# Kernel optimization log

Hardware: AMD Instinct MI355X
Metric: run time of the kernel (lower is better)

Reference implementation:

```python
import jax, jax.numpy as jnp
import numpy as np

B, S, D, H, ROT = 2, 2048, 2048, 16, 64
HD = D // H  # 128


def setup_inputs() -> dict:
    key = jax.random.key(0)
    ks = jax.random.split(key, 6)
    sc = 0.02
    return {
        "hidden_states": jax.random.normal(ks[0], (B, S, D), jnp.float32),
        "attention_mask": jnp.zeros((B, 1, 1, S), jnp.float32),  # HF additive mask; 0 == keep
        "position_ids": jnp.tile(jnp.arange(S, dtype=jnp.int32), (B, 1)),
        "Wq": jax.random.normal(ks[1], (D, D), jnp.float32) * sc,
        "Wk": jax.random.normal(ks[2], (D, D), jnp.float32) * sc,
        "Wv": jax.random.normal(ks[3], (D, D), jnp.float32) * sc,
        "Wo": jax.random.normal(ks[4], (D, D), jnp.float32) * sc,
        "norm_const": 0.5 * jnp.ones((1, H, 1, 1), jnp.float32),
    }


def _rotate_every_two(x):
    x1 = x[..., ::2]
    x2 = x[..., 1::2]
    return jnp.stack((-x2, x1), axis=-1).reshape(x.shape)


def _apply_rope(x, sin, cos):
    # x: [B,S,H,ROT]; sin/cos: [B,S,ROT//2] -> repeat_interleave(2) as in GPT-J
    sin2 = jnp.repeat(sin, 2, axis=-1)[:, :, None, :]
    cos2 = jnp.repeat(cos, 2, axis=-1)[:, :, None, :]
    return x * cos2 + _rotate_every_two(x) * sin2


def reference(hidden_states, attention_mask, position_ids, Wq, Wk, Wv, Wo, norm_const):
    # projections (nn.Linear, no bias): y = x @ W^T
    q = (hidden_states @ Wq.T).reshape(B, S, H, HD)
    k = (hidden_states @ Wk.T).reshape(B, S, H, HD)
    v = (hidden_states @ Wv.T).reshape(B, S, H, HD).transpose(0, 2, 1, 3)  # [B,H,S,HD]

    # GPT-J sinusoidal rotary on first ROT dims
    inv_freq = 1.0 / (10000.0 ** (jnp.arange(0, ROT, 2, dtype=jnp.float32) / ROT))
    ang = position_ids.astype(jnp.float32)[:, :, None] * inv_freq  # [B,S,ROT//2]
    sin, cos = jnp.sin(ang), jnp.cos(ang)
    q = jnp.concatenate([_apply_rope(q[..., :ROT], sin, cos), q[..., ROT:]], axis=-1)
    k = jnp.concatenate([_apply_rope(k[..., :ROT], sin, cos), k[..., ROT:]], axis=-1)
    q = q.transpose(0, 2, 1, 3)  # [B,H,S,HD]
    k = k.transpose(0, 2, 1, 3)

    # cosine attention: L2-normalize q and k (F.normalize, eps=1e-12)
    eps = 1e-12
    qn = q / jnp.clip(jnp.linalg.norm(q, axis=-1, keepdims=True), eps)
    kn = k / jnp.clip(jnp.linalg.norm(k, axis=-1, keepdims=True), eps)

    keep = attention_mask == 0                               # [B,1,1,S] bool
    causal = jnp.tril(jnp.ones((S, S), bool))[None, None]    # [1,1,S,S]
    # per-query count of visible keys -> value rescale with learned exponent
    counts = jnp.sum((causal & keep).astype(jnp.float32), axis=-1, keepdims=True)  # [B,1,S,1]
    expo = jax.nn.sigmoid(norm_const)                        # [1,H,1,1]
    v = v / jnp.clip(counts ** expo, 1.0)                    # [B,H,S,HD]

    keep_t = jnp.swapaxes(keep, -1, -2).astype(q.dtype)      # [B,1,S,1]
    qn = qn * keep_t
    kn = kn * keep_t
    v = v * keep_t

    attn = jnp.einsum('bhqd,bhkd->bhqk', qn, kn)             # cosine scores
    attn = jnp.where(causal, attn, 0.0)                      # causal zero-mask (no softmax)
    out = jnp.einsum('bhqk,bhkd->bhqd', attn, v)             # [B,H,S,HD]
    out = out.transpose(0, 2, 1, 3).reshape(B, S, D)
    return out @ Wo.T
```

## Files before the change

kernel.cpp:

```cpp
#include <hip/hip_runtime.h>
#include <hip/hip_bf16.h>

typedef __attribute__((ext_vector_type(8))) short bf16x8;
typedef __attribute__((ext_vector_type(4))) float f32x4;
typedef unsigned short u16;
typedef unsigned int u32;

constexpr int B = 2, S = 2048, D = 2048, H = 16, HD = 128, ROT = 64;
constexpr int NQKV = 3 * D;

__device__ __forceinline__ void gload16(const u16* g, u16* l)
{
    __builtin_amdgcn_global_load_lds((const __attribute__((address_space(1))) void*)g,
                                     (__attribute__((address_space(3))) void*)l, 16, 0, 0);
}

__device__ __forceinline__ float bf2f(u32 lo16) { return __uint_as_float(lo16 << 16); }

__global__ void fused_prep(const float* __restrict__ hs,
                           const float* __restrict__ Wq, const float* __restrict__ Wk,
                           const float* __restrict__ Wv, const float* __restrict__ Wo,
                           const float* __restrict__ mask, const int* __restrict__ pos,
                           const float* __restrict__ ncst,
                           u16* __restrict__ hs16, u16* __restrict__ wqkv16, u16* __restrict__ wo16,
                           float2* __restrict__ sc2, float* __restrict__ keep,
                           float* __restrict__ expo, float* __restrict__ counts)
{
    int bid = blockIdx.x, tid = threadIdx.x;
    if (bid < 1024) {
        const int total = 2097152 + 4 * 1048576;
        int idx = bid * 256 + tid;
        int stride = 1024 * 256;
        for (int i = idx; i < total; i += stride) {
            const float* src; u16* dst; int off;
            if (i < 2097152) { src = hs; dst = hs16; off = i; }
            else {
                int j = i - 2097152;
                int wsel = j >> 20; off = j & 1048575;
                src = wsel == 0 ? Wq : wsel == 1 ? Wk : wsel == 2 ? Wv : Wo;
                dst = wsel < 3 ? wqkv16 + (size_t)wsel * D * D : wo16;
            }
            float4 v = ((const float4*)src)[off];
            __hip_bfloat16 a = __float2bfloat16(v.x);
            __hip_bfloat16 b = __float2bfloat16(v.y);
            __hip_bfloat16 c = __float2bfloat16(v.z);
            __hip_bfloat16 d = __float2bfloat16(v.w);
            ushort4 o;
            o.x = *(u16*)&a; o.y = *(u16*)&b; o.z = *(u16*)&c; o.w = *(u16*)&d;
            ((ushort4*)dst)[off] = o;
        }
    } else if (bid < 1536) {
        int gid = (bid - 1024) * 256 + tid;
        int j = gid & 31;
        int bs = gid >> 5;
        float p = (float)pos[bs];
        float f = powf(10000.f, -(float)j / 32.f);
        float ang = p * f;
        sc2[gid] = make_float2(cosf(ang), sinf(ang));
        if (j == 0) keep[bs] = (mask[bs] == 0.f) ? 1.f : 0.f;
        if (gid < H) expo[gid] = 1.f / (1.f + expf(-ncst[gid]));
    } else {
        __shared__ float part[256];
        int b = bid - 1536, t = tid;
        float v[8];
        float s = 0.f;
        const float* mp = mask + b * S + t * 8;
#pragma unroll
        for (int i = 0; i < 8; ++i) { s += (mp[i] == 0.f) ? 1.f : 0.f; v[i] = s; }
        part[t] = s;
        __syncthreads();
        float off = 0.f;
        for (int j = 0; j < t; ++j) off += part[j];
        float* cp = counts + b * S + t * 8;
#pragma unroll
        for (int i = 0; i < 8; ++i) cp[i] = off + v[i];
    }
}


template <int CNT>
__device__ __forceinline__ void stage_op(const u16* __restrict__ G, int K,
                                         int trow0, int kt, u16* lbuf, int tid)
{
#pragma unroll
    for (int l = 0; l < CNT; ++l) {
        int idx = l * 512 + tid;
        int row = idx >> 2;
        int slot = idx & 3;
        int col8 = slot ^ ((row >> 1) & 3);
        const u16* g = G + (size_t)(trow0 + row) * K + kt * 32 + col8 * 8;
        u16* ld = lbuf + (size_t)(idx & ~63) * 8;
        gload16(g, ld);
    }
}

template <int BM, int BN, int CA, int CB, int MR, int NR, int BF16OUT>
__global__ __launch_bounds__(512, 2) void gemm32(
    const u16* __restrict__ A, const u16* __restrict__ Bm,
    float* __restrict__ Cf, u16* __restrict__ Cb, int N, int K, int ntn)
{
    __shared__ u16 As[3 * BM * 32];
    __shared__ u16 Bs[3 * BN * 32];
    const int tid = threadIdx.x;
    const int lane = tid & 63;
    const int w = tid >> 6;
    const int wm = w >> 2;
    const int wn = w & 3;
    const int l15 = lane & 15, l4 = lane >> 4;

    int nwg = gridDim.x;
    int bid = blockIdx.x;
    int cpx = nwg >> 3;
    int sbid = (bid & 7) * cpx + (bid >> 3);
    int bm = sbid / ntn, bn = sbid % ntn;
    const int bmrow = bm * BM, bnrow = bn * BN;

    f32x4 acc[MR][NR] = {};
    const int nk = K >> 5;

    stage_op<CA>(A, K, bmrow, 0, &As[0], tid);
    stage_op<CB>(Bm, K, bnrow, 0, &Bs[0], tid);
    stage_op<CA>(A, K, bmrow, 1, &As[BM * 32], tid);
    stage_op<CB>(Bm, K, bnrow, 1, &Bs[BN * 32], tid);

    int c0 = 0;
    for (int t = 0; t < nk; ++t) {
        const u16* ab = &As[c0 * BM * 32];
        const u16* bb = &Bs[c0 * BN * 32];
        if (t + 2 < nk) {
            int c2 = c0 + 2; if (c2 >= 3) c2 -= 3;
            stage_op<CA>(A, K, bmrow, t + 2, &As[c2 * BM * 32], tid);
            stage_op<CB>(Bm, K, bnrow, t + 2, &Bs[c2 * BN * 32], tid);
            asm volatile("s_waitcnt vmcnt(%0)" :: "i"(2 * (CA + CB)) : "memory");
        } else if (t + 1 < nk) {
            asm volatile("s_waitcnt vmcnt(%0)" :: "i"(CA + CB) : "memory");
        } else {
            asm volatile("s_waitcnt vmcnt(0)" ::: "memory");
        }
        __builtin_amdgcn_sched_barrier(0);
        __builtin_amdgcn_s_barrier();

        bf16x8 af[MR];
#pragma unroll
        for (int i = 0; i < MR; ++i) {
            int row = wm * (BM / 2) + i * 16 + l15;
            int slot = l4 ^ ((row >> 1) & 3);
            af[i] = *(const bf16x8*)(ab + row * 32 + slot * 8);
        }
#pragma unroll
        for (int n = 0; n < NR; ++n) {
            int brow = wn * (BN / 4) + n * 16 + l15;
            int bslot = l4 ^ ((brow >> 1) & 3);
            bf16x8 bf = *(const bf16x8*)(bb + brow * 32 + bslot * 8);
            __builtin_amdgcn_s_setprio(1);
#pragma unroll
            for (int i = 0; i < MR; ++i)
                acc[i][n] = __builtin_amdgcn_mfma_f32_16x16x32_bf16(af[i], bf, acc[i][n], 0, 0, 0);
            __builtin_amdgcn_s_setprio(0);
        }
        __builtin_amdgcn_sched_barrier(0);
        __builtin_amdgcn_s_barrier();
        c0 = (c0 + 1 == 3) ? 0 : c0 + 1;
    }

#pragma unroll
    for (int i = 0; i < MR; ++i) {
        int row = bmrow + wm * (BM / 2) + i * 16 + l4 * 4;
#pragma unroll
        for (int n = 0; n < NR; ++n) {
            int col = bnrow + wn * (BN / 4) + n * 16 + l15;
            f32x4 v = acc[i][n];
#pragma unroll
            for (int r = 0; r < 4; ++r) {
                if (BF16OUT) {
                    __hip_bfloat16 hv = __float2bfloat16(v[r]);
                    Cb[(size_t)(row + r) * N + col] = *(u16*)&hv;
                } else {
                    Cf[(size_t)(row + r) * N + col] = v[r];
                }
            }
        }
    }
}

__global__ void postproc_all(const u16* __restrict__ tmpb,
                             u16* __restrict__ qn, u16* __restrict__ kn, u16* __restrict__ vr,
                             const float2* __restrict__ sc2,
                             const float* __restrict__ keep, const float* __restrict__ counts,
                             const float* __restrict__ expo)
{
    int gw = (blockIdx.x * blockDim.x + threadIdx.x) >> 6;
    int lane = threadIdx.x & 63;
    if (gw >= B * S * H) return;
    int h = gw % H;
    int sb = gw / H;
    int s = sb % S;
    int b = sb / S;
    const u16* rowp = tmpb + (size_t)(b * S + s) * NQKV;
    u32 qv = *(const u32*)(rowp + h * 128 + lane * 2);
    u32 kv = *(const u32*)(rowp + D + h * 128 + lane * 2);
    u32 vv = *(const u32*)(rowp + 2 * D + h * 128 + lane * 2);
    float q0 = bf2f(qv & 0xffff), q1 = bf2f(qv >> 16);
    float k0 = bf2f(kv & 0xffff), k1 = bf2f(kv >> 16);
    float v0 = bf2f(vv & 0xffff), v1 = bf2f(vv >> 16);
    if (lane < 32) {
        float2 cs = sc2[(b * S + s) * 32 + lane];
        float nq0 = q0 * cs.x - q1 * cs.y, nq1 = q1 * cs.x + q0 * cs.y;
        float nk0 = k0 * cs.x - k1 * cs.y, nk1 = k1 * cs.x + k0 * cs.y;
        q0 = nq0; q1 = nq1; k0 = nk0; k1 = nk1;
    }
    float sq = q0 * q0 + q1 * q1;
    float sk = k0 * k0 + k1 * k1;
#pragma unroll
    for (int o = 1; o < 64; o <<= 1) {
        sq += __shfl_xor(sq, o, 64);
        sk += __shfl_xor(sk, o, 64);
    }
    float kf = keep[b * S + s];
    float scq = kf / fmaxf(sqrtf(sq), 1e-12f);
    float sck = kf / fmaxf(sqrtf(sk), 1e-12f);
    float cnt = counts[b * S + s];
    float e = expo[h];
    float scv = kf / fmaxf(powf(cnt, e), 1.0f);

    __hip_bfloat16 a0 = __float2bfloat16(q0 * scq), a1 = __float2bfloat16(q1 * scq);
    __hip_bfloat16 b0 = __float2bfloat16(k0 * sck), b1 = __float2bfloat16(k1 * sck);
    __hip_bfloat16 c0 = __float2bfloat16(v0 * scv), c1 = __float2bfloat16(v1 * scv);
    size_t obase = ((size_t)(b * H + h) * S + s) * 128 + lane * 2;
    *(u32*)(qn + obase) = (u32)*(u16*)&a0 | ((u32)*(u16*)&a1 << 16);
    *(u32*)(kn + obase) = (u32)*(u16*)&b0 | ((u32)*(u16*)&b1 << 16);
    *(u32*)(vr + obase) = (u32)*(u16*)&c0 | ((u32)*(u16*)&c1 << 16);
}

__global__ __launch_bounds__(256) void chunk_state(
    const u16* __restrict__ kn, const u16* __restrict__ vr, u16* __restrict__ T16)
{
    __shared__ u16 As[128][72];
    __shared__ u16 Bs[128][72];
    int tid = threadIdx.x, lane = tid & 63, w = tid >> 6;
    int wm = w >> 1, wn = w & 1;
    int c = blockIdx.x, bh = blockIdx.y;
    const int l15 = lane & 15, l4 = lane >> 4;
    size_t base = (size_t)bh * S * 128;
    f32x4 acc[4][4] = {};

    for (int t = 0; t < 2; ++t) {
#pragma unroll
        for (int i = 0; i < 4; ++i) {
            int q = tid + i * 256;
            int r = q >> 4, c16 = q & 15;
            uint4 v = *(const uint4*)(vr + base + (size_t)(c * 128 + t * 64 + r) * 128 + c16 * 8);
            const u16* pv = (const u16*)&v;
#pragma unroll
            for (int j = 0; j < 8; ++j) As[c16 * 8 + j][r] = pv[j];
        }
#pragma unroll
        for (int i = 0; i < 4; ++i) {
            int q = tid + i * 256;
            int r = q >> 4, c16 = q & 15;
            uint4 v = *(const uint4*)(kn + base + (size_t)(c * 128 + t * 64 + r) * 128 + c16 * 8);
            const u16* pv = (const u16*)&v;
#pragma unroll
            for (int j = 0; j < 8; ++j) Bs[c16 * 8 + j][r] = pv[j];
        }
        __syncthreads();
#pragma unroll
        for (int tt = 0; tt < 2; ++tt) {
            bf16x8 a[4], b[4];
#pragma unroll
            for (int m = 0; m < 4; ++m)
                a[m] = *(const bf16x8*)(&As[wm * 64 + m * 16 + l15][tt * 32 + l4 * 8]);
#pragma unroll
            for (int n = 0; n < 4; ++n)
                b[n] = *(const bf16x8*)(&Bs[wn * 64 + n * 16 + l15][tt * 32 + l4 * 8]);
#pragma unroll
            for (int m = 0; m < 4; ++m)
#pragma unroll
                for (int n = 0; n < 4; ++n)
                    acc[m][n] = __builtin_amdgcn_mfma_f32_16x16x32_bf16(a[m], b[n], acc[m][n], 0, 0, 0);
        }
        __syncthreads();
    }
#pragma unroll
    for (int m = 0; m < 4; ++m) {
        int row = wm * 64 + m * 16 + l4 * 4;
#pragma unroll
        for (int n = 0; n < 4; ++n) {
            int col = wn * 64 + n * 16 + l15;
#pragma unroll
            for (int r = 0; r < 4; ++r) {
                __hip_bfloat16 hv = __float2bfloat16(acc[m][n][r]);
                T16[((size_t)(bh * 16 + c) * 128 + row + r) * 128 + col] = *(u16*)&hv;
            }
        }
    }
}

__global__ void prefix_state(const u16* __restrict__ T16, u16* __restrict__ P16)
{
    int g = blockIdx.x * blockDim.x + threadIdx.x;
    int bh = g >> 11;
    int i8 = (g & 2047) * 8;
    const u16* tp = T16 + (size_t)bh * 16 * 16384 + i8;
    u16* pp = P16 + (size_t)bh * 16 * 16384 + i8;
    float run[8] = {};
    for (int c = 0; c < 16; ++c) {
        u16 ob[8];
#pragma unroll
        for (int j = 0; j < 8; ++j) { __hip_bfloat16 hv = __float2bfloat16(run[j]); ob[j] = *(u16*)&hv; }
        *(uint4*)(pp + (size_t)c * 16384) = *(uint4*)ob;
        uint4 tv = *(const uint4*)(tp + (size_t)c * 16384);
        const u16* tvp = (const u16*)&tv;
#pragma unroll
        for (int j = 0; j < 8; ++j) run[j] += bf2f(tvp[j]);
    }
}

__global__ __launch_bounds__(256, 2) void attn2(
    const u16* __restrict__ qn, const u16* __restrict__ kn,
    const u16* __restrict__ vr, const u16* __restrict__ P16, u16* __restrict__ ao)
{
    __shared__ u16 KN[64][136];
    __shared__ u16 VT[128][72];
    __shared__ u16 SC[128][72];
    int tid = threadIdx.x, lane = tid & 63, w = tid >> 6;
    int c = blockIdx.x, bh = blockIdx.y;
    int b = bh >> 4, h = bh & 15;
    const int l15 = lane & 15, l4 = lane >> 4;
    size_t base = (size_t)bh * S * 128;
    const u16* Pp = P16 + (size_t)(bh * 16 + c) * 16384;

    bf16x8 qa[2][4];
#pragma unroll
    for (int m = 0; m < 2; ++m)
#pragma unroll
        for (int t = 0; t < 4; ++t) {
            int row = c * 128 + w * 32 + m * 16 + l15;
            qa[m][t] = *(const bf16x8*)(qn + base + (size_t)row * 128 + t * 32 + l4 * 8);
        }

    f32x4 acc[2][8] = {};

#pragma unroll
    for (int pt = 0; pt < 2; ++pt) {
#pragma unroll
        for (int i = 0; i < 4; ++i) {
            int q = tid + i * 256;
            int r = q >> 3, c8 = q & 7;
            uint4 v = *(const uint4*)(Pp + (size_t)r * 128 + pt * 64 + c8 * 8);
            *(uint4*)(&VT[r][c8 * 8]) = v;
        }
        __syncthreads();
#pragma unroll
        for (int tt = 0; tt < 2; ++tt) {
            bf16x8 pb[8];
#pragma unroll
            for (int n = 0; n < 8; ++n)
                pb[n] = *(const bf16x8*)(&VT[n * 16 + l15][tt * 32 + l4 * 8]);
#pragma unroll
            for (int m = 0; m < 2; ++m)
#pragma unroll
                for (int n = 0; n < 8; ++n)
                    acc[m][n] = __builtin_amdgcn_mfma_f32_16x16x32_bf16(qa[m][pt * 2 + tt], pb[n], acc[m][n], 0, 0, 0);
        }
        __syncthreads();
    }

    for (int kt2 = 0; kt2 < 2; ++kt2) {
#pragma unroll
        for (int i = 0; i < 4; ++i) {
            int q = tid + i * 256;
            int r = q >> 4, c8 = q & 15;
            uint4 v = *(const uint4*)(kn + base + (size_t)(c * 128 + kt2 * 64 + r) * 128 + c8 * 8);
            *(uint4*)(&KN[r][c8 * 8]) = v;
        }
#pragma unroll
        for (int i = 0; i < 4; ++i) {
            int q = tid + i * 256;
            int r = q >> 4, c16 = q & 15;
            uint4 v = *(const uint4*)(vr + base + (size_t)(c * 128 + kt2 * 64 + r) * 128 + c16 * 8);
            const u16* pv = (const u16*)&v;
#pragma unroll
            for (int j = 0; j < 8; ++j) VT[c16 * 8 + j][r] = pv[j];
        }
        __syncthreads();
        f32x4 sacc[2][4] = {};
#pragma unroll
        for (int t = 0; t < 4; ++t) {
            bf16x8 kb[4];
#pragma unroll
            for (int n = 0; n < 4; ++n)
                kb[n] = *(const bf16x8*)(&KN[n * 16 + l15][t * 32 + l4 * 8]);
#pragma unroll
            for (int m = 0; m < 2; ++m)
#pragma unroll
                for (int n = 0; n < 4; ++n)
                    sacc[m][n] = __builtin_amdgcn_mfma_f32_16x16x32_bf16(qa[m][t], kb[n], sacc[m][n], 0, 0, 0);
        }
#pragma unroll
        for (int m = 0; m < 2; ++m)
#pragma unroll
            for (int n = 0; n < 4; ++n)
#pragma unroll
                for (int r = 0; r < 4; ++r) {
                    int rowl = w * 32 + m * 16 + l4 * 4 + r;
                    int coll = n * 16 + l15;
                    int kl = kt2 * 64 + coll;
                    float val = (kl <= rowl) ? sacc[m][n][r] : 0.f;
                    __hip_bfloat16 hv = __float2bfloat16(val);
                    SC[rowl][coll] = *(u16*)&hv;
                }
#pragma unroll
        for (int t = 0; t < 2; ++t) {
            bf16x8 sa[2], vb[8];
#pragma unroll
            for (int m = 0; m < 2; ++m)
                sa[m] = *(const bf16x8*)(&SC[w * 32 + m * 16 + l15][t * 32 + l4 * 8]);
#pragma unroll
            for (int n = 0; n < 8; ++n)
                vb[n] = *(const bf16x8*)(&VT[n * 16 + l15][t * 32 + l4 * 8]);
#pragma unroll
            for (int m = 0; m < 2; ++m)
#pragma unroll
                for (int n = 0; n < 8; ++n)
                    acc[m][n] = __builtin_amdgcn_mfma_f32_16x16x32_bf16(sa[m], vb[n], acc[m][n], 0, 0, 0);
        }
        __syncthreads();
    }

#pragma unroll
    for (int m = 0; m < 2; ++m)
#pragma unroll
        for (int n = 0; n < 8; ++n)
#pragma unroll
            for (int r = 0; r < 4; ++r) {
                int srow = c * 128 + w * 32 + m * 16 + l4 * 4 + r;
                int d = n * 16 + l15;
                __hip_bfloat16 hv = __float2bfloat16(acc[m][n][r]);
                ao[(size_t)(b * S + srow) * D + h * 128 + d] = *(u16*)&hv;
            }
}

extern "C" void kernel_launch(void* const* d_in, const int* in_sizes, int n_in,
                              void* d_out, int out_size, void* d_ws, size_t ws_size,
                              hipStream_t stream)
{
    const float* hs = (const float*)d_in[0];
    const float* mask = (const float*)d_in[1];
    const int* pos = (const int*)d_in[2];
    const float* Wq = (const float*)d_in[3];
    const float* Wk = (const float*)d_in[4];
    const float* Wv = (const float*)d_in[5];
    const float* Wo = (const float*)d_in[6];
    const float* ncst = (const float*)d_in[7];
    float* out = (float*)d_out;

    char* ws = (char*)d_ws;
    size_t off = 0;
    auto alloc = [&](size_t bytes) {
        size_t o = off;
        off += (bytes + 255) & ~(size_t)255;
        return o;
    };
    u16* hs16 = (u16*)(ws + alloc((size_t)B * S * D * 2));
    u16* wqkv16 = (u16*)(ws + alloc((size_t)NQKV * D * 2));
    u16* wo16 = (u16*)(ws + alloc((size_t)D * D * 2));
    u16* tmpb = (u16*)(ws + alloc((size_t)B * S * NQKV * 2));
    u16* qn16 = (u16*)(ws + alloc((size_t)B * S * D * 2));
    u16* kn16 = (u16*)(ws + alloc((size_t)B * S * D * 2));
    u16* vr16 = (u16*)(ws + alloc((size_t)B * S * D * 2));
    float2* sc2 = (float2*)(ws + alloc((size_t)B * S * 32 * 8));
    float* keep = (float*)(ws + alloc((size_t)B * S * 4));
    float* counts = (float*)(ws + alloc((size_t)B * S * 4));
    float* expo = (float*)(ws + alloc(64));
    u16* ao16 = tmpb;
    u16* T16 = tmpb + (size_t)8388608;
    u16* P16 = tmpb + (size_t)16777216;

    fused_prep<<<1538, 256, 0, stream>>>(hs, Wq, Wk, Wv, Wo, mask, pos, ncst,
                                         hs16, wqkv16, wo16, sc2, keep, expo, counts);

    gemm32<256, 384, 2, 3, 8, 6, 1><<<256, 512, 0, stream>>>(
        hs16, wqkv16, nullptr, tmpb, NQKV, D, NQKV / 384);

    postproc_all<<<(B * S * H) / 4, 256, 0, stream>>>(tmpb, qn16, kn16, vr16,
                                                      sc2, keep, counts, expo);

    dim3 gc(S / 128, B * H);
    chunk_state<<<gc, 256, 0, stream>>>(kn16, vr16, T16);
    prefix_state<<<256, 256, 0, stream>>>(T16, P16);
    attn2<<<gc, 256, 0, stream>>>(qn16, kn16, vr16, P16, ao16);

    gemm32<128, 256, 1, 2, 4, 4, 0><<<256, 512, 0, stream>>>(
        ao16, wo16, out, nullptr, D, D, D / 256);
}
```

Measured before the change: 275.1 us.

## Switch GEMMs to 64-wide K tiles with double-buffered LDS

```diff
diff --git a/kernel.cpp b/kernel.cpp
--- a/kernel.cpp
+++ b/kernel.cpp
@@ -79,28 +79,28 @@
 
 
 template <int CNT>
-__device__ __forceinline__ void stage_op(const u16* __restrict__ G, int K,
-                                         int trow0, int kt, u16* lbuf, int tid)
+__device__ __forceinline__ void stage64(const u16* __restrict__ G, int K,
+                                        int trow0, int kt, u16* lbuf, int tid)
 {
 #pragma unroll
     for (int l = 0; l < CNT; ++l) {
         int idx = l * 512 + tid;
-        int row = idx >> 2;
-        int slot = idx & 3;
-        int col8 = slot ^ ((row >> 1) & 3);
-        const u16* g = G + (size_t)(trow0 + row) * K + kt * 32 + col8 * 8;
+        int row = idx >> 3;
+        int slot = idx & 7;
+        int col8 = slot ^ (row & 7);
+        const u16* g = G + (size_t)(trow0 + row) * K + kt * 64 + col8 * 8;
         u16* ld = lbuf + (size_t)(idx & ~63) * 8;
         gload16(g, ld);
     }
 }
 
 template <int BM, int BN, int CA, int CB, int MR, int NR, int BF16OUT>
-__global__ __launch_bounds__(512, 2) void gemm32(
+__global__ __launch_bounds__(512, 1) void gemm64(
     const u16* __restrict__ A, const u16* __restrict__ Bm,
     float* __restrict__ Cf, u16* __restrict__ Cb, int N, int K, int ntn)
 {
-    __shared__ u16 As[3 * BM * 32];
-    __shared__ u16 Bs[3 * BN * 32];
+    __shared__ u16 As[2 * BM * 64];
+    __shared__ u16 Bs[2 * BN * 64];
     const int tid = threadIdx.x;
     const int lane = tid & 63;
     const int w = tid >> 6;
@@ -116,23 +116,17 @@
     const int bmrow = bm * BM, bnrow = bn * BN;
 
     f32x4 acc[MR][NR] = {};
-    const int nk = K >> 5;
-
-    stage_op<CA>(A, K, bmrow, 0, &As[0], tid);
-    stage_op<CB>(Bm, K, bnrow, 0, &Bs[0], tid);
-    stage_op<CA>(A, K, bmrow, 1, &As[BM * 32], tid);
-    stage_op<CB>(Bm, K, bnrow, 1, &Bs[BN * 32], tid);
-
-    int c0 = 0;
+    const int nk = K >> 6;
+
+    stage64<CA>(A, K, bmrow, 0, &As[0], tid);
+    stage64<CB>(Bm, K, bnrow, 0, &Bs[0], tid);
+
     for (int t = 0; t < nk; ++t) {
-        const u16* ab = &As[c0 * BM * 32];
-        const u16* bb = &Bs[c0 * BN * 32];
-        if (t + 2 < nk) {
-            int c2 = c0 + 2; if (c2 >= 3) c2 -= 3;
-            stage_op<CA>(A, K, bmrow, t + 2, &As[c2 * BM * 32], tid);
-            stage_op<CB>(Bm, K, bnrow, t + 2, &Bs[c2 * BN * 32], tid);
-            asm volatile("s_waitcnt vmcnt(%0)" :: "i"(2 * (CA + CB)) : "memory");
-        } else if (t + 1 < nk) {
+        const u16* ab = &As[(t & 1) * BM * 64];
+        const u16* bb = &Bs[(t & 1) * BN * 64];
+        if (t + 1 < nk) {
+            stage64<CA>(A, K, bmrow, t + 1, &As[((t + 1) & 1) * BM * 64], tid);
+            stage64<CB>(Bm, K, bnrow, t + 1, &Bs[((t + 1) & 1) * BN * 64], tid);
             asm volatile("s_waitcnt vmcnt(%0)" :: "i"(CA + CB) : "memory");
         } else {
             asm volatile("s_waitcnt vmcnt(0)" ::: "memory");
@@ -140,27 +134,29 @@
         __builtin_amdgcn_sched_barrier(0);
         __builtin_amdgcn_s_barrier();
 
-        bf16x8 af[MR];
-#pragma unroll
-        for (int i = 0; i < MR; ++i) {
-            int row = wm * (BM / 2) + i * 16 + l15;
-            int slot = l4 ^ ((row >> 1) & 3);
-            af[i] = *(const bf16x8*)(ab + row * 32 + slot * 8);
-        }
-#pragma unroll
-        for (int n = 0; n < NR; ++n) {
-            int brow = wn * (BN / 4) + n * 16 + l15;
-            int bslot = l4 ^ ((brow >> 1) & 3);
-            bf16x8 bf = *(const bf16x8*)(bb + brow * 32 + bslot * 8);
-            __builtin_amdgcn_s_setprio(1);
-#pragma unroll
-            for (int i = 0; i < MR; ++i)
-                acc[i][n] = __builtin_amdgcn_mfma_f32_16x16x32_bf16(af[i], bf, acc[i][n], 0, 0, 0);
-            __builtin_amdgcn_s_setprio(0);
+#pragma unroll
+        for (int tt = 0; tt < 2; ++tt) {
+            bf16x8 af[MR];
+#pragma unroll
+            for (int i = 0; i < MR; ++i) {
+                int row = wm * (BM / 2) + i * 16 + l15;
+                int slot = (tt * 4 + l4) ^ (row & 7);
+                af[i] = *(const bf16x8*)(ab + row * 64 + slot * 8);
+            }
+#pragma unroll
+            for (int n = 0; n < NR; ++n) {
+                int brow = wn * (BN / 4) + n * 16 + l15;
+                int bslot = (tt * 4 + l4) ^ (brow & 7);
+                bf16x8 bf = *(const bf16x8*)(bb + brow * 64 + bslot * 8);
+                __builtin_amdgcn_s_setprio(1);
+#pragma unroll
+                for (int i = 0; i < MR; ++i)
+                    acc[i][n] = __builtin_amdgcn_mfma_f32_16x16x32_bf16(af[i], bf, acc[i][n], 0, 0, 0);
+                __builtin_amdgcn_s_setprio(0);
+            }
         }
         __builtin_amdgcn_sched_barrier(0);
         __builtin_amdgcn_s_barrier();
-        c0 = (c0 + 1 == 3) ? 0 : c0 + 1;
     }
 
 #pragma unroll
@@ -480,7 +476,7 @@
     fused_prep<<<1538, 256, 0, stream>>>(hs, Wq, Wk, Wv, Wo, mask, pos, ncst,
                                          hs16, wqkv16, wo16, sc2, keep, expo, counts);
 
-    gemm32<256, 384, 2, 3, 8, 6, 1><<<256, 512, 0, stream>>>(
+    gemm64<256, 384, 4, 6, 8, 6, 1><<<256, 512, 0, stream>>>(
         hs16, wqkv16, nullptr, tmpb, NQKV, D, NQKV / 384);
 
     postproc_all<<<(B * S * H) / 4, 256, 0, stream>>>(tmpb, qn16, kn16, vr16,
@@ -491,6 +487,6 @@
     prefix_state<<<256, 256, 0, stream>>>(T16, P16);
     attn2<<<gc, 256, 0, stream>>>(qn16, kn16, vr16, P16, ao16);
 
-    gemm32<128, 256, 1, 2, 4, 4, 0><<<256, 512, 0, stream>>>(
+    gemm64<128, 256, 2, 4, 4, 4, 0><<<256, 512, 0, stream>>>(
         ao16, wo16, out, nullptr, D, D, D / 256);
 }
```

After: 263.8 us (median of 2 runs). -4.1%, faster.
